# Optimization experiments

Measured on AMD Instinct MI355X. Metric: run time of the kernel, lower is better.

The kernel has to match this reference:

```python
import jax, jax.numpy as jnp
import numpy as np

EPS = 1e-6
LOG_2PI = float(np.log(2.0 * np.pi))


def setup_inputs() -> dict:
    key = jax.random.key(0)
    k1, k2 = jax.random.split(key)
    z = jax.random.normal(k1, (8, 32, 256, 256), dtype=jnp.float32)
    g = jax.random.uniform(k2, (8, 5, 256, 256), dtype=jnp.float32)
    return {"z": z, "g": g}


def _gmm_energy(z, g):
    b, c, h, w = z.shape
    k = g.shape[1]
    hw = h * w
    zf = z.reshape(b, c, hw)
    gf = g.reshape(b, k, hw)

    # phi: mean responsibility per component, [b, k]
    phi = jnp.sum(gf, axis=2) / hw

    # mu: weighted mean, then l2-normalized over channels, [b, k, c]
    gz = jnp.einsum('bkn,bcn->bkc', gf, zf)
    mu = gz / (jnp.sum(gf, axis=2, keepdims=True) + EPS)
    mu = mu / (EPS + jnp.linalg.norm(mu, axis=-1, keepdims=True))

    # centered data, [b, k, c, hw]
    z_mu = zf[:, None, :, :] - mu[..., None]

    # cov: in the source the g-weighting algebraically cancels
    # (sum(g)*M / sum(g) where M = z_mu @ z_mu.T), so cov = z_mu @ z_mu.T
    cov = jnp.einsum('bkcn,bkdn->bkcd', z_mu, z_mu)  # [b, k, c, c]
    # get_pd: add diag(clamp(diag, 1e-6)) (doubles the diagonal, floored)
    d = jnp.maximum(jnp.diagonal(cov, axis1=-2, axis2=-1), EPS)  # [b, k, c]
    cov = cov + jnp.eye(c, dtype=cov.dtype) * d[..., None, :]
    # l2norm over dims (0,1) of each [c,c] block = Frobenius normalization
    fro = jnp.sqrt(jnp.sum(cov * cov, axis=(-2, -1), keepdims=True))
    cov = cov / (EPS + fro)

    # energy: MVN log-prob of every pixel under each (b,k) Gaussian,
    # with phi (NOT log phi, faithful to source) added before logsumexp.
    L = jnp.linalg.cholesky(cov)  # [b, k, c, c]
    y = jax.scipy.linalg.solve_triangular(L, z_mu, lower=True)  # [b, k, c, hw]
    maha = jnp.sum(y * y, axis=2)  # [b, k, hw]
    logdet = 2.0 * jnp.sum(jnp.log(jnp.diagonal(L, axis1=-2, axis2=-1)), axis=-1)  # [b, k]
    log_prob = -0.5 * (c * LOG_2PI + maha) - 0.5 * logdet[..., None]  # [b, k, hw]
    weighted = log_prob + phi[..., None]
    log_sum = jax.scipy.special.logsumexp(weighted, axis=-1)  # [b, k]
    energy = -jnp.mean(log_sum) / hw
    return energy


def reference(z, g):
    return _gmm_energy(z, g)
```

## Files before the change

kernel.cpp:

```cpp
#include <hip/hip_runtime.h>
#include <math.h>

constexpr int B = 8, C = 32, K = 5, HW = 65536;
constexpr int K1B  = 64;
constexpr int K1PX = HW / K1B;
constexpr int NIT  = K1PX / 128;
constexpr int K3PX = 256;
constexpr int K3BLK = HW / K3PX;
constexpr int NPART = K3BLK * 4;
constexpr float NEG_HALF_C_LOG2PI_F = -29.406033062549518f;

typedef __attribute__((ext_vector_type(8))) short bf16x8;
typedef __attribute__((ext_vector_type(4))) float f32x4;

__device__ inline unsigned short f2bf(float f) {
  unsigned int u = __float_as_uint(f);
  return (unsigned short)((u + 0x7fffu + ((u >> 16) & 1u)) >> 16);
}
__device__ inline float bf2f(unsigned short h) {
  return __uint_as_float(((unsigned int)h) << 16);
}

__global__ __launch_bounds__(256) void k1_gram(const float* __restrict__ z,
                                               const float* __restrict__ g,
                                               float* __restrict__ part) {
  __shared__ __align__(16) unsigned short xs[96 * 136];
  unsigned int* xsu = (unsigned int*)xs;
  const int tid  = threadIdx.x;
  const int lane = tid & 63;
  const int w    = tid >> 6;
  const int b    = blockIdx.x / K1B;
  const int blk  = blockIdx.x % K1B;
  const int px0  = blk * K1PX;

  for (int idx = tid; idx < 22 * 64; idx += 256) {
    int rr  = idx >> 6;
    int row = (rr < 11) ? (37 + rr) : (85 + rr - 11);
    xsu[row * 68 + (idx & 63)] = (row == 37) ? 0x3f803f80u : 0u;
  }

  f32x4 a00 = {0.f,0.f,0.f,0.f}, a10 = {0.f,0.f,0.f,0.f}, a11 = {0.f,0.f,0.f,0.f};
  f32x4 a20 = {0.f,0.f,0.f,0.f}, a21 = {0.f,0.f,0.f,0.f}, a22 = {0.f,0.f,0.f,0.f};

  float2 pre[10];
#pragma unroll
  for (int j = 0; j < 10; ++j) {
    int r = w + 4 * j;
    if (r < 37) {
      const float* src = (r < 32) ? (z + (size_t)(b * C + r) * HW)
                                  : (g + (size_t)(b * K + (r - 32)) * HW);
      pre[j] = ((const float2*)(src + px0))[lane];
    }
  }

  const int lm = lane & 15, q = lane >> 4;
  const int co = w * 32 + q * 8;

  for (int it = 0; it < NIT; ++it) {
    __syncthreads();
#pragma unroll
    for (int j = 0; j < 10; ++j) {
      int r = w + 4 * j;
      if (r < 37) {
        unsigned short hx = f2bf(pre[j].x), hy = f2bf(pre[j].y);
        float lx = pre[j].x - bf2f(hx);
        float ly = pre[j].y - bf2f(hy);
        xsu[r * 68 + lane]        = (unsigned int)hx | ((unsigned int)hy << 16);
        xsu[(r + 48) * 68 + lane] = (unsigned int)f2bf(lx) | ((unsigned int)f2bf(ly) << 16);
      }
    }
    __syncthreads();
    if (it + 1 < NIT) {
#pragma unroll
      for (int j = 0; j < 10; ++j) {
        int r = w + 4 * j;
        if (r < 37) {
          const float* src = (r < 32) ? (z + (size_t)(b * C + r) * HW)
                                      : (g + (size_t)(b * K + (r - 32)) * HW);
          pre[j] = ((const float2*)(src + px0 + (it + 1) * 128))[lane];
        }
      }
    }
    bf16x8 f0h = *(const bf16x8*)&xs[(0  + lm) * 136 + co];
    bf16x8 f1h = *(const bf16x8*)&xs[(16 + lm) * 136 + co];
    bf16x8 f2h = *(const bf16x8*)&xs[(32 + lm) * 136 + co];
    bf16x8 f0l = *(const bf16x8*)&xs[(48 + lm) * 136 + co];
    bf16x8 f1l = *(const bf16x8*)&xs[(64 + lm) * 136 + co];
    bf16x8 f2l = *(const bf16x8*)&xs[(80 + lm) * 136 + co];
#define MF(d, x, y) d = __builtin_amdgcn_mfma_f32_16x16x32_bf16(x, y, d, 0, 0, 0)
    MF(a00, f0h, f0h); MF(a00, f0h, f0l); MF(a00, f0l, f0h);
    MF(a10, f1h, f0h); MF(a10, f1h, f0l); MF(a10, f1l, f0h);
    MF(a11, f1h, f1h); MF(a11, f1h, f1l); MF(a11, f1l, f1h);
    MF(a20, f2h, f0h); MF(a20, f2h, f0l); MF(a20, f2l, f0h);
    MF(a21, f2h, f1h); MF(a21, f2h, f1l); MF(a21, f2l, f1h);
    MF(a22, f2h, f2h); MF(a22, f2h, f2l); MF(a22, f2l, f2h);
#undef MF
  }

  __syncthreads();
  float* fb = (float*)xs;
#pragma unroll
  for (int rr = 0; rr < 4; ++rr) {
    fb[((w * 6 + 0) * 4 + rr) * 64 + lane] = a00[rr];
    fb[((w * 6 + 1) * 4 + rr) * 64 + lane] = a10[rr];
    fb[((w * 6 + 2) * 4 + rr) * 64 + lane] = a11[rr];
    fb[((w * 6 + 3) * 4 + rr) * 64 + lane] = a20[rr];
    fb[((w * 6 + 4) * 4 + rr) * 64 + lane] = a21[rr];
    fb[((w * 6 + 5) * 4 + rr) * 64 + lane] = a22[rr];
  }
  __syncthreads();
  float* po = part + (size_t)blockIdx.x * 1536;
#pragma unroll
  for (int t = 0; t < 6; ++t) {
    int sl = (tid >> 6), ln = (tid & 63);
    float v = fb[((0 * 6 + t) * 4 + sl) * 64 + ln] + fb[((1 * 6 + t) * 4 + sl) * 64 + ln]
            + fb[((2 * 6 + t) * 4 + sl) * 64 + ln] + fb[((3 * 6 + t) * 4 + sl) * 64 + ln];
    po[t * 256 + tid] = v;
  }
}

__global__ void k1b_reduce(const float* __restrict__ part, float* __restrict__ gram) {
  const int b = blockIdx.x / 6, t = blockIdx.x % 6;
  const int tid = threadIdx.x;
  const int rr = tid >> 6, lane = tid & 63;
  const int m = (lane >> 4) * 4 + rr, n = lane & 15;
  const int TI[6] = {0, 1, 1, 2, 2, 2};
  const int TJ[6] = {0, 0, 1, 0, 1, 2};
  double s = 0.0;
#pragma unroll 8
  for (int blk = 0; blk < K1B; ++blk)
    s += (double)part[(size_t)(b * K1B + blk) * 1536 + t * 256 + tid];
  int gr = TI[t] * 16 + m, gc = TJ[t] * 16 + n;
  if (gr < 40 && gc < 40) {
    gram[b * 1600 + gr * 40 + gc] = (float)s;
    gram[b * 1600 + gc * 40 + gr] = (float)s;
  }
}

__global__ __launch_bounds__(64) void k2_setup(const float* __restrict__ gram,
                                               unsigned short* __restrict__ ABout,
                                               float* __restrict__ vout,
                                               float* __restrict__ cterm,
                                               unsigned int* __restrict__ counter) {
  const int b = blockIdx.x / K, k = blockIdx.x % K;
  const float* G = gram + b * 1600;
  const int lane = threadIdx.x;
  const int j32 = lane & 31;
  __shared__ float Amat[32][33];
  __shared__ float mus[32];
  if (blockIdx.x == 0 && lane == 0) *counter = 0u;

  const float sg = G[37 * 40 + 32 + k];
  float muj = G[(32 + k) * 40 + j32] / (sg + 1e-6f);
  const float szj = G[37 * 40 + j32];
  float nrm = muj * muj;
#pragma unroll
  for (int d = 1; d < 32; d <<= 1) nrm += __shfl_xor(nrm, d, 64);
  muj *= 1.f / (1e-6f + sqrtf(nrm));
  if (lane < 32) mus[lane] = muj;

  float col[32];
#pragma unroll
  for (int i = 0; i < 32; ++i) {
    const float mu_i = __shfl(muj, i, 64);
    const float sz_i = __shfl(szj, i, 64);
    float cv = G[i * 40 + j32] - mu_i * szj - muj * sz_i + 65536.f * mu_i * muj;
    if (i == lane) cv += fmaxf(cv, 1e-6f);
    col[i] = cv;
  }
  float fs = 0.f;
#pragma unroll
  for (int i = 0; i < 32; ++i) fs = fmaf(col[i], col[i], fs);
#pragma unroll
  for (int d = 1; d < 32; d <<= 1) fs += __shfl_xor(fs, d, 64);
  const float fsc = 1.f / (1e-6f + sqrtf(fs));
#pragma unroll
  for (int i = 0; i < 32; ++i) col[i] *= fsc;

  float sown = 0.f, dcap = 1.f;
#pragma unroll
  for (int j = 0; j < 32; ++j) {
    float dd = __shfl(col[j], j, 64);
    dd = fmaxf(dd, 1e-30f);
    const float s = 1.f / sqrtf(dd);
    if (lane == j) { sown = s; dcap = dd; }
    const float f = (lane > j) ? col[j] * s : 0.f;
#pragma unroll
    for (int i = j + 1; i < 32; ++i) {
      const float cji = __shfl(col[i], j, 64) * s;
      col[i] = fmaf(-cji, f, col[i]);
    }
  }

  float Lc[32];
#pragma unroll
  for (int i = 0; i < 32; ++i) Lc[i] = col[i] * sown;

  float x[32];
#pragma unroll
  for (int i = 0; i < 32; ++i) {
    float t0 = (lane == i) ? 1.f : 0.f, t1 = 0.f, t2 = 0.f, t3 = 0.f;
#pragma unroll
    for (int qq = 0; qq < i; ++qq) {
      const float lq = __shfl(Lc[i], qq, 64);
      const float p = lq * x[qq];
      if ((qq & 3) == 0) t0 -= p;
      else if ((qq & 3) == 1) t1 -= p;
      else if ((qq & 3) == 2) t2 -= p;
      else t3 -= p;
    }
    const float Lii = __shfl(Lc[i], i, 64);
    x[i] = ((t0 + t1) + (t2 + t3)) / Lii;
  }

  if (lane < 32) {
#pragma unroll
    for (int i = 0; i < 32; ++i) Amat[i][lane] = x[i];
  }
  __syncthreads();

  if (lane < 32) {
    float t = 0.f;
    for (int d2 = 0; d2 <= lane; ++d2) t = fmaf(Amat[lane][d2], mus[d2], t);
    vout[(b * K + k) * 32 + lane] = t;
  }

  float lg = 0.5f * logf(dcap);
#pragma unroll
  for (int d = 1; d < 32; d <<= 1) lg += __shfl_xor(lg, d, 64);
  if (lane == 0)
    cterm[b * K + k] = NEG_HALF_C_LOG2PI_F - lg + sg / 65536.f;

  unsigned short* Ao = ABout + (size_t)(b * K + k) * 2048;
#pragma unroll
  for (int e = lane; e < 1024; e += 64) {
    const int m = e >> 5, d2 = e & 31;
    const float a = Amat[m][d2];
    const unsigned int u = __float_as_uint(a);
    const float hf = __uint_as_float(u & 0xffff0000u);
    Ao[e] = (unsigned short)(u >> 16);
    Ao[1024 + e] = (unsigned short)(__float_as_uint(a - hf) >> 16);
  }
}

__global__ __launch_bounds__(256) void k3_maha(const float* __restrict__ z,
                                               const unsigned short* __restrict__ AB,
                                               const float* __restrict__ vglob,
                                               float2* __restrict__ partials) {
  __shared__ __align__(16) unsigned short zt[K3PX * 40];
  const int tid  = threadIdx.x;
  const int lane = tid & 63;
  const int w    = tid >> 6;
  const int b    = blockIdx.x / K3BLK;
  const int chb  = blockIdx.x % K3BLK;
  const int px0  = chb * K3PX;

  {
    const float* zb = z + (size_t)b * C * HW + px0 + 4 * lane;
    float4 rv[8];
#pragma unroll
    for (int i = 0; i < 8; ++i)
      rv[i] = *(const float4*)(zb + (size_t)(w * 8 + i) * HW);
#pragma unroll
    for (int p = 0; p < 4; ++p) {
      unsigned int hh[4];
#pragma unroll
      for (int i = 0; i < 8; i += 2) {
        const float a0 = (&rv[i].x)[p], a1 = (&rv[i + 1].x)[p];
        hh[i >> 1] = (unsigned int)f2bf(a0) | ((unsigned int)f2bf(a1) << 16);
      }
      *(uint4*)&zt[(4 * lane + p) * 40 + w * 8] = make_uint4(hh[0], hh[1], hh[2], hh[3]);
    }
  }
  __syncthreads();

  const int lm = lane & 15, q = lane >> 4;
  bf16x8 Ah[K][2], Al[K][2];
  f32x4 Ci[K][2];
#pragma unroll
  for (int k = 0; k < K; ++k) {
    const unsigned short* Abase = AB + (size_t)(b * K + k) * 2048;
    const float* vb = vglob + (size_t)(b * K + k) * 32;
#pragma unroll
    for (int mt = 0; mt < 2; ++mt) {
      const int m = mt * 16 + lm;
      Ah[k][mt] = *(const bf16x8*)(Abase + m * 32 + q * 8);
      Al[k][mt] = *(const bf16x8*)(Abase + 1024 + m * 32 + q * 8);
#pragma unroll
      for (int r = 0; r < 4; ++r)
        Ci[k][mt][r] = -vb[mt * 16 + q * 4 + r];
    }
  }

  float mm[K], ss[K];
#pragma unroll
  for (int k = 0; k < K; ++k) { mm[k] = -1e30f; ss[k] = 0.f; }

#pragma unroll
  for (int nt = 0; nt < 4; ++nt) {
    const int px = w * 64 + nt * 16 + lm;
    bf16x8 zh = *(const bf16x8*)&zt[px * 40 + q * 8];
#pragma unroll
    for (int k = 0; k < K; ++k) {
      float acc = 0.f;
#pragma unroll
      for (int mt = 0; mt < 2; ++mt) {
        f32x4 y = Ci[k][mt];
        y = __builtin_amdgcn_mfma_f32_16x16x32_bf16(Ah[k][mt], zh, y, 0, 0, 0);
        y = __builtin_amdgcn_mfma_f32_16x16x32_bf16(Al[k][mt], zh, y, 0, 0, 0);
#pragma unroll
        for (int r = 0; r < 4; ++r) acc = fmaf(y[r], y[r], acc);
      }
      acc += __shfl_xor(acc, 16, 64);
      acc += __shfl_xor(acc, 32, 64);
      const float L = -0.5f * acc;
      const float nm = fmaxf(mm[k], L);
      ss[k] = ss[k] * __expf(mm[k] - nm) + __expf(L - nm);
      mm[k] = nm;
    }
  }
#pragma unroll
  for (int k = 0; k < K; ++k) {
#pragma unroll
    for (int d = 1; d < 16; d <<= 1) {
      float mo = __shfl_xor(mm[k], d, 64);
      float so = __shfl_xor(ss[k], d, 64);
      float nm = fmaxf(mm[k], mo);
      ss[k] = ss[k] * __expf(mm[k] - nm) + so * __expf(mo - nm);
      mm[k] = nm;
    }
    if (lane == 0)
      partials[((size_t)(b * K + k) * K3BLK + chb) * 4 + w] = make_float2(mm[k], ss[k]);
  }
}

__global__ __launch_bounds__(64) void k4_final(const float2* __restrict__ partials,
                                               const float* __restrict__ cterm,
                                               float* __restrict__ lsebuf,
                                               unsigned int* __restrict__ counter,
                                               float* __restrict__ out) {
  const int bk = blockIdx.x;
  const int lane = threadIdx.x;
  const float2* p = partials + (size_t)bk * NPART;
  float M = -1e30f, S = 0.f;
#pragma unroll 4
  for (int i = lane; i < NPART; i += 64) {
    const float2 qq = p[i];
    const float nm = fmaxf(M, qq.x);
    S = S * __expf(M - nm) + qq.y * __expf(qq.x - nm);
    M = nm;
  }
#pragma unroll
  for (int d = 1; d < 64; d <<= 1) {
    const float mo = __shfl_xor(M, d, 64);
    const float so = __shfl_xor(S, d, 64);
    const float nm = fmaxf(M, mo);
    S = S * __expf(M - nm) + so * __expf(mo - nm);
    M = nm;
  }
  __shared__ int last;
  if (lane == 0) {
    atomicExch(&lsebuf[bk], M + logf(S) + cterm[bk]);
    __threadfence();
    last = (atomicAdd(counter, 1u) == 39u) ? 1 : 0;
  }
  __syncthreads();
  if (last) {
    const float v = (lane < 40) ? atomicAdd(&lsebuf[lane], 0.f) : 0.f;
    double dv = (double)v;
#pragma unroll
    for (int d = 1; d < 64; d <<= 1) dv += __shfl_xor(dv, d, 64);
    if (lane == 0) out[0] = (float)(-dv / (40.0 * 65536.0));
  }
}

extern "C" void kernel_launch(void* const* d_in, const int* in_sizes, int n_in,
                              void* d_out, int out_size, void* d_ws, size_t ws_size,
                              hipStream_t stream) {
  const float* z = (const float*)d_in[0];
  const float* g = (const float*)d_in[1];
  float* out = (float*)d_out;

  float2* part3 = (float2*)d_ws;
  float*  part1 = (float*)(part3 + 40 * NPART);
  unsigned short* AB = (unsigned short*)(part1 + (size_t)(B * K1B) * 1536);
  float*  gram   = (float*)(AB + 40 * 2048);
  float*  vv     = gram + B * 1600;
  float*  ct     = vv + B * K * 32;
  float*  lsebuf = ct + B * K;
  unsigned int* counter = (unsigned int*)(lsebuf + 40);

  k1_gram<<<B * K1B, 256, 0, stream>>>(z, g, part1);
  k1b_reduce<<<B * 6, 256, 0, stream>>>(part1, gram);
  k2_setup<<<B * K, 64, 0, stream>>>(gram, AB, vv, ct, counter);
  k3_maha<<<B * K3BLK, 256, 0, stream>>>(z, AB, vv, part3);
  k4_final<<<B * K, 64, 0, stream>>>(part3, ct, lsebuf, counter, out);
}
```

Before: 167.0 us.

## Drop split-bf16 Gram precision, fuse partial reduction into setup, use plain-sum logsumexp

The Gram kernel now uses a single bf16 rounding instead of a hi/lo split, cutting its MFMA work to a third and halving the LDS staging. The separate partial-reduction kernel is folded into k2_setup, where each block re-reduces its batch's partials in float into shared memory. The Mahalanobis kernel now sums exp(-0.5*maha) directly, with no running max, and k4 takes the log of that sum. The trade-offs are lower Gram precision in the covariance and Cholesky path, possible underflow of the exp sum, and five-fold redundant partial reads in k2.

```diff
diff --git a/kernel.cpp b/kernel.cpp
--- a/kernel.cpp
+++ b/kernel.cpp
@@ -16,9 +16,6 @@
 __device__ inline unsigned short f2bf(float f) {
   unsigned int u = __float_as_uint(f);
   return (unsigned short)((u + 0x7fffu + ((u >> 16) & 1u)) >> 16);
-}
-__device__ inline float bf2f(unsigned short h) {
-  return __uint_as_float(((unsigned int)h) << 16);
 }
 
 __global__ __launch_bounds__(256) void k1_gram(const float* __restrict__ z,
@@ -33,9 +30,8 @@
   const int blk  = blockIdx.x % K1B;
   const int px0  = blk * K1PX;
 
-  for (int idx = tid; idx < 22 * 64; idx += 256) {
-    int rr  = idx >> 6;
-    int row = (rr < 11) ? (37 + rr) : (85 + rr - 11);
+  for (int idx = tid; idx < 11 * 64; idx += 256) {
+    int row = 37 + (idx >> 6);
     xsu[row * 68 + (idx & 63)] = (row == 37) ? 0x3f803f80u : 0u;
   }
 
@@ -61,13 +57,8 @@
 #pragma unroll
     for (int j = 0; j < 10; ++j) {
       int r = w + 4 * j;
-      if (r < 37) {
-        unsigned short hx = f2bf(pre[j].x), hy = f2bf(pre[j].y);
-        float lx = pre[j].x - bf2f(hx);
-        float ly = pre[j].y - bf2f(hy);
-        xsu[r * 68 + lane]        = (unsigned int)hx | ((unsigned int)hy << 16);
-        xsu[(r + 48) * 68 + lane] = (unsigned int)f2bf(lx) | ((unsigned int)f2bf(ly) << 16);
-      }
+      if (r < 37)
+        xsu[r * 68 + lane] = (unsigned int)f2bf(pre[j].x) | ((unsigned int)f2bf(pre[j].y) << 16);
     }
     __syncthreads();
     if (it + 1 < NIT) {
@@ -81,19 +72,12 @@
         }
       }
     }
-    bf16x8 f0h = *(const bf16x8*)&xs[(0  + lm) * 136 + co];
-    bf16x8 f1h = *(const bf16x8*)&xs[(16 + lm) * 136 + co];
-    bf16x8 f2h = *(const bf16x8*)&xs[(32 + lm) * 136 + co];
-    bf16x8 f0l = *(const bf16x8*)&xs[(48 + lm) * 136 + co];
-    bf16x8 f1l = *(const bf16x8*)&xs[(64 + lm) * 136 + co];
-    bf16x8 f2l = *(const bf16x8*)&xs[(80 + lm) * 136 + co];
+    bf16x8 f0 = *(const bf16x8*)&xs[(0  + lm) * 136 + co];
+    bf16x8 f1 = *(const bf16x8*)&xs[(16 + lm) * 136 + co];
+    bf16x8 f2 = *(const bf16x8*)&xs[(32 + lm) * 136 + co];
 #define MF(d, x, y) d = __builtin_amdgcn_mfma_f32_16x16x32_bf16(x, y, d, 0, 0, 0)
-    MF(a00, f0h, f0h); MF(a00, f0h, f0l); MF(a00, f0l, f0h);
-    MF(a10, f1h, f0h); MF(a10, f1h, f0l); MF(a10, f1l, f0h);
-    MF(a11, f1h, f1h); MF(a11, f1h, f1l); MF(a11, f1l, f1h);
-    MF(a20, f2h, f0h); MF(a20, f2h, f0l); MF(a20, f2l, f0h);
-    MF(a21, f2h, f1h); MF(a21, f2h, f1l); MF(a21, f2l, f1h);
-    MF(a22, f2h, f2h); MF(a22, f2h, f2l); MF(a22, f2l, f2h);
+    MF(a00, f0, f0); MF(a10, f1, f0); MF(a11, f1, f1);
+    MF(a20, f2, f0); MF(a21, f2, f1); MF(a22, f2, f2);
 #undef MF
   }
 
@@ -119,36 +103,53 @@
   }
 }
 
-__global__ void k1b_reduce(const float* __restrict__ part, float* __restrict__ gram) {
-  const int b = blockIdx.x / 6, t = blockIdx.x % 6;
-  const int tid = threadIdx.x;
-  const int rr = tid >> 6, lane = tid & 63;
-  const int m = (lane >> 4) * 4 + rr, n = lane & 15;
-  const int TI[6] = {0, 1, 1, 2, 2, 2};
-  const int TJ[6] = {0, 0, 1, 0, 1, 2};
-  double s = 0.0;
-#pragma unroll 8
-  for (int blk = 0; blk < K1B; ++blk)
-    s += (double)part[(size_t)(b * K1B + blk) * 1536 + t * 256 + tid];
-  int gr = TI[t] * 16 + m, gc = TJ[t] * 16 + n;
-  if (gr < 40 && gc < 40) {
-    gram[b * 1600 + gr * 40 + gc] = (float)s;
-    gram[b * 1600 + gc * 40 + gr] = (float)s;
-  }
-}
-
-__global__ __launch_bounds__(64) void k2_setup(const float* __restrict__ gram,
+__global__ __launch_bounds__(64) void k2_setup(const float* __restrict__ part,
                                                unsigned short* __restrict__ ABout,
                                                float* __restrict__ vout,
                                                float* __restrict__ cterm,
                                                unsigned int* __restrict__ counter) {
   const int b = blockIdx.x / K, k = blockIdx.x % K;
-  const float* G = gram + b * 1600;
   const int lane = threadIdx.x;
   const int j32 = lane & 31;
+  __shared__ float gram[1600];
   __shared__ float Amat[32][33];
   __shared__ float mus[32];
   if (blockIdx.x == 0 && lane == 0) *counter = 0u;
+
+  {
+    f32x4 accs[6];
+#pragma unroll
+    for (int j = 0; j < 6; ++j) accs[j] = (f32x4){0.f, 0.f, 0.f, 0.f};
+    const float* pb = part + (size_t)(b * K1B) * 1536 + 4 * lane;
+#pragma unroll 4
+    for (int blk = 0; blk < K1B; ++blk) {
+      const float* pp = pb + (size_t)blk * 1536;
+#pragma unroll
+      for (int j = 0; j < 6; ++j) {
+        const f32x4 v = *(const f32x4*)(pp + j * 256);
+#pragma unroll
+        for (int c = 0; c < 4; ++c) accs[j][c] += v[c];
+      }
+    }
+    const int TI[6] = {0, 1, 1, 2, 2, 2};
+    const int TJ[6] = {0, 0, 1, 0, 1, 2};
+#pragma unroll
+    for (int j = 0; j < 6; ++j) {
+#pragma unroll
+      for (int c = 0; c < 4; ++c) {
+        const int idx = 4 * lane + c;
+        const int rr = idx >> 6, ln = idx & 63;
+        const int m = (ln >> 4) * 4 + rr, n = ln & 15;
+        const int gr = TI[j] * 16 + m, gc = TJ[j] * 16 + n;
+        if (gr < 40 && gc < 40) {
+          gram[gr * 40 + gc] = accs[j][c];
+          gram[gc * 40 + gr] = accs[j][c];
+        }
+      }
+    }
+  }
+  __syncthreads();
+  const float* G = gram;
 
   const float sg = G[37 * 40 + 32 + k];
   float muj = G[(32 + k) * 40 + j32] / (sg + 1e-6f);
@@ -246,7 +247,7 @@
 __global__ __launch_bounds__(256) void k3_maha(const float* __restrict__ z,
                                                const unsigned short* __restrict__ AB,
                                                const float* __restrict__ vglob,
-                                               float2* __restrict__ partials) {
+                                               float* __restrict__ partials) {
   __shared__ __align__(16) unsigned short zt[K3PX * 40];
   const int tid  = threadIdx.x;
   const int lane = tid & 63;
@@ -292,9 +293,9 @@
     }
   }
 
-  float mm[K], ss[K];
-#pragma unroll
-  for (int k = 0; k < K; ++k) { mm[k] = -1e30f; ss[k] = 0.f; }
+  float sacc[K];
+#pragma unroll
+  for (int k = 0; k < K; ++k) sacc[k] = 0.f;
 
 #pragma unroll
   for (int nt = 0; nt < 4; ++nt) {
@@ -313,54 +314,35 @@
       }
       acc += __shfl_xor(acc, 16, 64);
       acc += __shfl_xor(acc, 32, 64);
-      const float L = -0.5f * acc;
-      const float nm = fmaxf(mm[k], L);
-      ss[k] = ss[k] * __expf(mm[k] - nm) + __expf(L - nm);
-      mm[k] = nm;
+      sacc[k] += __expf(-0.5f * acc);
     }
   }
 #pragma unroll
   for (int k = 0; k < K; ++k) {
-#pragma unroll
-    for (int d = 1; d < 16; d <<= 1) {
-      float mo = __shfl_xor(mm[k], d, 64);
-      float so = __shfl_xor(ss[k], d, 64);
-      float nm = fmaxf(mm[k], mo);
-      ss[k] = ss[k] * __expf(mm[k] - nm) + so * __expf(mo - nm);
-      mm[k] = nm;
-    }
+    float s = sacc[k];
+#pragma unroll
+    for (int d = 1; d < 16; d <<= 1) s += __shfl_xor(s, d, 64);
     if (lane == 0)
-      partials[((size_t)(b * K + k) * K3BLK + chb) * 4 + w] = make_float2(mm[k], ss[k]);
-  }
-}
-
-__global__ __launch_bounds__(64) void k4_final(const float2* __restrict__ partials,
+      partials[((size_t)(b * K + k) * K3BLK + chb) * 4 + w] = s;
+  }
+}
+
+__global__ __launch_bounds__(64) void k4_final(const float* __restrict__ partials,
                                                const float* __restrict__ cterm,
                                                float* __restrict__ lsebuf,
                                                unsigned int* __restrict__ counter,
                                                float* __restrict__ out) {
   const int bk = blockIdx.x;
   const int lane = threadIdx.x;
-  const float2* p = partials + (size_t)bk * NPART;
-  float M = -1e30f, S = 0.f;
+  const float* p = partials + (size_t)bk * NPART;
+  float S = 0.f;
 #pragma unroll 4
-  for (int i = lane; i < NPART; i += 64) {
-    const float2 qq = p[i];
-    const float nm = fmaxf(M, qq.x);
-    S = S * __expf(M - nm) + qq.y * __expf(qq.x - nm);
-    M = nm;
-  }
-#pragma unroll
-  for (int d = 1; d < 64; d <<= 1) {
-    const float mo = __shfl_xor(M, d, 64);
-    const float so = __shfl_xor(S, d, 64);
-    const float nm = fmaxf(M, mo);
-    S = S * __expf(M - nm) + so * __expf(mo - nm);
-    M = nm;
-  }
+  for (int i = lane; i < NPART; i += 64) S += p[i];
+#pragma unroll
+  for (int d = 1; d < 64; d <<= 1) S += __shfl_xor(S, d, 64);
   __shared__ int last;
   if (lane == 0) {
-    atomicExch(&lsebuf[bk], M + logf(S) + cterm[bk]);
+    atomicExch(&lsebuf[bk], logf(fmaxf(S, 1e-37f)) + cterm[bk]);
     __threadfence();
     last = (atomicAdd(counter, 1u) == 39u) ? 1 : 0;
   }
@@ -381,18 +363,16 @@
   const float* g = (const float*)d_in[1];
   float* out = (float*)d_out;
 
-  float2* part3 = (float2*)d_ws;
-  float*  part1 = (float*)(part3 + 40 * NPART);
+  float*  part3 = (float*)d_ws;
+  float*  part1 = part3 + 40 * NPART;
   unsigned short* AB = (unsigned short*)(part1 + (size_t)(B * K1B) * 1536);
-  float*  gram   = (float*)(AB + 40 * 2048);
-  float*  vv     = gram + B * 1600;
+  float*  vv     = (float*)(AB + 40 * 2048);
   float*  ct     = vv + B * K * 32;
   float*  lsebuf = ct + B * K;
   unsigned int* counter = (unsigned int*)(lsebuf + 40);
 
   k1_gram<<<B * K1B, 256, 0, stream>>>(z, g, part1);
-  k1b_reduce<<<B * 6, 256, 0, stream>>>(part1, gram);
-  k2_setup<<<B * K, 64, 0, stream>>>(gram, AB, vv, ct, counter);
+  k2_setup<<<B * K, 64, 0, stream>>>(part1, AB, vv, ct, counter);
   k3_maha<<<B * K3BLK, 256, 0, stream>>>(z, AB, vv, part3);
   k4_final<<<B * K, 64, 0, stream>>>(part3, ct, lsebuf, counter, out);
 }
```

Measured after the change: 171.0 us. 2.4% more time.
